# Kernel tuning notes

Hardware: AMD Instinct MI355X
Metric: run time of the kernel (lower is better)

The kernel has to match this reference:

```python
import jax, jax.numpy as jnp
import numpy as np

DECAY = 0.999
EPS = 1e-05
COMMIT = 0.25


def _layer_norm(x, g, b, eps=1e-5):
    mu = x.mean(-1, keepdims=True)
    var = ((x - mu) ** 2).mean(-1, keepdims=True)
    return (x - mu) * jax.lax.rsqrt(var + eps) * g + b


def setup_inputs() -> dict:
    key = jax.random.key(0)
    ks = jax.random.split(key, 8)
    B, T, D, M, H = 8, 4096, 512, 1024, 512
    init_bound = 1.0 / 512
    embedding = jax.random.uniform(ks[0], (M, D), jnp.float32, -init_bound, init_bound)
    return {
        "dense_x": jax.random.normal(ks[1], (B, T, D), jnp.float32),
        "dense_padding_mask": jax.random.randint(ks[2], (B, T), 0, 2).astype(bool),
        "labels": jax.random.randint(ks[3], (B, T), 0, M),
        "embedding": embedding,
        "ema_count": jnp.zeros((M,), jnp.float32),
        "ema_weight": embedding,
        "ln1_g": jnp.ones((D,), jnp.float32),
        "ln1_b": jnp.zeros((D,), jnp.float32),
        "W1": jax.random.normal(ks[4], (D, H), jnp.float32) * (1.0 / np.sqrt(D)),
        "ln2_g": jnp.ones((H,), jnp.float32),
        "ln2_b": jnp.zeros((H,), jnp.float32),
        "W2": jax.random.normal(ks[5], (H, M), jnp.float32) * (1.0 / np.sqrt(H)),
    }


def reference(dense_x, dense_padding_mask, labels, embedding, ema_count, ema_weight,
              ln1_g, ln1_b, W1, ln2_g, ln2_b, W2):
    B, T, D = dense_x.shape
    M = embedding.shape[0]
    N = B * T

    # ---- VQ codebook (EMA) ----
    x_flat = jax.lax.stop_gradient(dense_x).reshape(N, D)
    distances = (jnp.sum(embedding ** 2, axis=1)[None, :]
                 + jnp.sum(x_flat ** 2, axis=1, keepdims=True)
                 - 2.0 * (x_flat @ embedding.T))
    indices = jnp.argmin(distances, axis=-1)  # [N]
    quantized = embedding[indices].reshape(B, T, D)

    # EMA codebook update (training path); encodings.sum(0) and encodings.T @ x
    # expressed as scatter-adds instead of materializing [N, M] one-hot.
    counts = jnp.zeros((M,), dense_x.dtype).at[indices].add(1.0)
    new_count = DECAY * ema_count + (1.0 - DECAY) * counts
    n = jnp.sum(new_count)
    new_count = (new_count + EPS) / (n + M * EPS) * n
    dw = jnp.zeros((M, D), dense_x.dtype).at[indices].add(x_flat)
    new_weight = DECAY * ema_weight + (1.0 - DECAY) * dw
    new_embedding = new_weight / new_count[:, None]

    e_latent_loss = (dense_x - jax.lax.stop_gradient(quantized)) ** 2  # [B,T,D]
    vq_loss = COMMIT * e_latent_loss
    quantized_st = dense_x + jax.lax.stop_gradient(quantized - dense_x)

    avg_probs = counts / N
    perplexity = jnp.exp(-jnp.sum(avg_probs * jnp.log(avg_probs + 1e-10)))

    # ---- decoder: LN -> ReLU -> Linear -> LN -> ReLU -> Linear ----
    h = jax.nn.relu(_layer_norm(dense_x, ln1_g, ln1_b)) @ W1      # [B,T,H]
    logits = jax.nn.relu(_layer_norm(h, ln2_g, ln2_b)) @ W2       # [B,T,M]

    # ---- cross-entropy with ignore_index=-1 (padding) ----
    lab = jnp.where(dense_padding_mask, -1, labels)
    valid = lab >= 0
    safe = jnp.where(valid, lab, 0)
    logp = jax.nn.log_softmax(logits, axis=-1)
    ce = -jnp.take_along_axis(logp, safe[..., None], axis=-1)[..., 0]
    recon_loss = jnp.where(valid, ce, 0.0)

    loss = recon_loss + vq_loss.sum(-1)  # [B,T]
    return quantized_st, loss, perplexity, new_embedding, new_count, new_weight
```

## Files before the change

kernel.cpp:

```cpp
#include <hip/hip_runtime.h>


#define N_TOK 32768
#define WAITV(n) __builtin_amdgcn_s_waitcnt(0x0F70 | (n))
#define BAR() __builtin_amdgcn_s_barrier()

typedef __attribute__((ext_vector_type(8))) short short8;
typedef _Float16 half8 __attribute__((ext_vector_type(8)));
typedef __attribute__((ext_vector_type(4))) float f32x4;

__device__ __forceinline__ f32x4 mfma16(short8 a, short8 b, f32x4 c) {
    return __builtin_amdgcn_mfma_f32_16x16x32_bf16(a, b, c, 0, 0, 0);
}
__device__ __forceinline__ f32x4 mfma16h(half8 a, half8 b, f32x4 c) {
    return __builtin_amdgcn_mfma_f32_16x16x32_f16(a, b, c, 0, 0, 0);
}

__device__ __forceinline__ void gl_lds16(const unsigned short* g, char* l) {
    __builtin_amdgcn_global_load_lds(
        (const __attribute__((address_space(1))) void*)g,
        (__attribute__((address_space(3))) void*)l, 16, 0, 0);
}

__device__ __forceinline__ unsigned short f2bf(float x) {
    unsigned u = __float_as_uint(x);
    u += 0x7fffu + ((u >> 16) & 1u);
    return (unsigned short)(u >> 16);
}
__device__ __forceinline__ float bf2f(unsigned short h) {
    return __uint_as_float(((unsigned)h) << 16);
}
__device__ __forceinline__ unsigned short f2h(float x) {
    union { _Float16 h; unsigned short u; } c;
    c.h = (_Float16)x;
    return c.u;
}
__device__ __forceinline__ float h2f(unsigned short u) {
    union { _Float16 h; unsigned short u; } c;
    c.u = u;
    return (float)c.h;
}

__device__ __forceinline__ float waveSum(float v) {
#pragma unroll
    for (int off = 32; off > 0; off >>= 1) v += __shfl_down(v, off, 64);
    return v;
}
__device__ __forceinline__ float xorSum(float v) {
#pragma unroll
    for (int off = 1; off < 64; off <<= 1) v += __shfl_xor(v, off);
    return v;
}

__global__ __launch_bounds__(256) void prep_x_kernel(
        const float* __restrict__ X, const float* __restrict__ g,
        const float* __restrict__ b, unsigned short* __restrict__ Xf,
        unsigned short* __restrict__ A1, unsigned long long* __restrict__ minpack) {
    int tid = threadIdx.x;
    if (tid < 4) minpack[(blockIdx.x << 2) + tid] = ~0ULL;
    int lane = tid & 63;
    int n = (blockIdx.x << 2) + (tid >> 6);
    const float* row = X + ((size_t)n << 9);
    float v[8]; float s = 0.f, ss = 0.f;
#pragma unroll
    for (int i = 0; i < 8; ++i) { v[i] = row[lane + (i << 6)]; s += v[i]; ss += v[i] * v[i]; }
    s = xorSum(s); ss = xorSum(ss);
    float mu = s * (1.f / 512.f);
    float rs = rsqrtf(ss * (1.f / 512.f) - mu * mu + 1e-5f);
#pragma unroll
    for (int i = 0; i < 8; ++i) {
        int c = lane + (i << 6);
        size_t o = ((size_t)n << 9) + c;
        float x = v[i];
        Xf[o] = f2h(x);
        float a = fmaxf((x - mu) * rs * g[c] + b[c], 0.f);
        A1[o] = f2bf(a);
    }
}

__global__ __launch_bounds__(256) void prep_h_kernel(
        const unsigned short* __restrict__ Hb, const float* __restrict__ g,
        const float* __restrict__ b, unsigned short* __restrict__ A2) {
    int lane = threadIdx.x & 63;
    int n = (blockIdx.x << 2) + (threadIdx.x >> 6);
    const unsigned short* row = Hb + ((size_t)n << 9);
    float v[8]; float s = 0.f, ss = 0.f;
#pragma unroll
    for (int i = 0; i < 8; ++i) { v[i] = bf2f(row[lane + (i << 6)]); s += v[i]; ss += v[i] * v[i]; }
    s = xorSum(s); ss = xorSum(ss);
    float mu = s * (1.f / 512.f);
    float rs = rsqrtf(ss * (1.f / 512.f) - mu * mu + 1e-5f);
#pragma unroll
    for (int i = 0; i < 8; ++i) {
        int c = lane + (i << 6);
        float a = fmaxf((v[i] - mu) * rs * g[c] + b[c], 0.f);
        A2[((size_t)n << 9) + c] = f2bf(a);
    }
}

__global__ __launch_bounds__(256) void prep_e_kernel(
        const float* __restrict__ E, unsigned short* __restrict__ Ehf,
        unsigned short* __restrict__ Elf, float* __restrict__ e_sq,
        int* __restrict__ izero) {
    if (blockIdx.x < 8) izero[(blockIdx.x << 8) + threadIdx.x] = 0;
    int lane = threadIdx.x & 63;
    int m = (blockIdx.x << 2) + (threadIdx.x >> 6);
    const float* row = E + ((size_t)m << 9);
    float ss = 0.f;
#pragma unroll
    for (int i = 0; i < 8; ++i) {
        int c = lane + (i << 6);
        float x = row[c];
        ss += x * x;
        float xs = x * 512.f;
        unsigned short h = f2h(xs);
        size_t o = ((size_t)m << 9) + c;
        Ehf[o] = h;
        Elf[o] = f2h(xs - h2f(h));
    }
    ss = xorSum(ss);
    if (lane == 0) e_sq[m] = ss * 512.f;
}

__global__ __launch_bounds__(256) void prep_wt_kernel(
        const float* __restrict__ W1, const float* __restrict__ W2,
        unsigned short* __restrict__ W1T, unsigned short* __restrict__ W2T) {
    __shared__ float t[32][33];
    int bx = blockIdx.x;
    const float* W = (bx < 16) ? W1 : W2;
    unsigned short* WT = (bx < 16) ? W1T : W2T;
    int Nw = (bx < 16) ? 512 : 1024;
    int n0 = ((bx < 16) ? bx : (bx - 16)) << 5, k0 = blockIdx.y << 5;
    int tx = threadIdx.x & 31, ty = threadIdx.x >> 5;
#pragma unroll
    for (int l = 0; l < 4; ++l)
        t[ty + (l << 3)][tx] = W[(size_t)(k0 + ty + (l << 3)) * Nw + n0 + tx];
    __syncthreads();
#pragma unroll
    for (int l = 0; l < 4; ++l)
        WT[(((size_t)(n0 + ty + (l << 3))) << 9) + k0 + tx] = f2bf(t[tx][ty + (l << 3)]);
}

__device__ __forceinline__ unsigned long long packDist(float d, int m) {
    unsigned u = __float_as_uint(d);
    u = (u & 0x80000000u) ? ~u : (u | 0x80000000u);
    return ((unsigned long long)u << 32) | (unsigned)m;
}

__global__ __launch_bounds__(256) void dist_mfma_kernel(
        const unsigned short* __restrict__ Xf,
        const unsigned short* __restrict__ Ehf, const unsigned short* __restrict__ Elf,
        const float* __restrict__ e_sq, unsigned long long* __restrict__ minpack) {
    __shared__ __align__(16) short L[2][3][4096];
    int tid = threadIdx.x, lane = tid & 63, w = tid >> 6;
    int quad = lane >> 4, lanelo = lane & 15;
    int wm = w >> 1, wn = w & 1;
    int bid = blockIdx.x, xcd = bid & 7, s = bid >> 3;
    int row0 = (((s >> 3) << 3) | xcd) << 7;
    int m0 = (s & 7) << 7;

    int srow = ((w & 1) << 6) + lane;
    int skoff = (w >> 1) << 4;
    const unsigned short* pX = Xf  + (((size_t)(row0 + srow)) << 9) + skoff;
    const unsigned short* pH = Ehf + (((size_t)(m0  + srow)) << 9) + skoff;
    const unsigned short* pL = Elf + (((size_t)(m0  + srow)) << 9) + skoff;
    char* ldsB = (char*)&L[0][0][0] + ((w >> 1) << 12) + ((w & 1) << 10) + (lane << 4);
    const char* ra  = (const char*)&L[0][0][0] + (quad << 11) + (((wm << 6) + lanelo) << 4);
    const char* rbh = (const char*)&L[0][1][0] + (quad << 11) + (((wn << 6) + lanelo) << 4);

    f32x4 acc[4][4];
#pragma unroll
    for (int i = 0; i < 4; ++i)
#pragma unroll
        for (int j = 0; j < 4; ++j) acc[i][j] = 0.f;

    gl_lds16(pX, ldsB);            gl_lds16(pX + 8, ldsB + 2048);
    gl_lds16(pH, ldsB + 8192);     gl_lds16(pH + 8, ldsB + 10240);
    gl_lds16(pL, ldsB + 16384);    gl_lds16(pL + 8, ldsB + 18432);

#pragma unroll
    for (int it = 0; it < 16; ++it) {
        const int cb = it & 1;
        if (it < 15) {
            const unsigned short* sX = pX + ((it + 1) << 5);
            const unsigned short* sH = pH + ((it + 1) << 5);
            const unsigned short* sL = pL + ((it + 1) << 5);
            char* d = ldsB + (cb ^ 1) * 24576;
            gl_lds16(sX, d);           gl_lds16(sX + 8, d + 2048);
            gl_lds16(sH, d + 8192);    gl_lds16(sH + 8, d + 10240);
            gl_lds16(sL, d + 16384);   gl_lds16(sL + 8, d + 18432);
            WAITV(6);
        } else {
            WAITV(0);
        }
        BAR();
        const char* A  = ra  + cb * 24576;
        const char* Bh = rbh + cb * 24576;
        half8 av[4], bh[4], bl[4];
#pragma unroll
        for (int i = 0; i < 4; ++i) av[i] = *(const half8*)(A + (i << 8));
#pragma unroll
        for (int j = 0; j < 4; ++j) {
            bh[j] = *(const half8*)(Bh + (j << 8));
            bl[j] = *(const half8*)(Bh + 8192 + (j << 8));
        }
#pragma unroll
        for (int i = 0; i < 4; ++i)
#pragma unroll
            for (int j = 0; j < 4; ++j) acc[i][j] = mfma16h(av[i], bh[j], acc[i][j]);
#pragma unroll
        for (int i = 0; i < 4; ++i)
#pragma unroll
            for (int j = 0; j < 4; ++j) acc[i][j] = mfma16h(av[i], bl[j], acc[i][j]);
        BAR();
    }

    float esq[4];
#pragma unroll
    for (int j = 0; j < 4; ++j) esq[j] = e_sq[m0 + (wn << 6) + (j << 4) + lanelo];
#pragma unroll
    for (int i = 0; i < 4; ++i)
#pragma unroll
        for (int r = 0; r < 4; ++r) {
            unsigned long long best = ~0ULL;
#pragma unroll
            for (int j = 0; j < 4; ++j) {
                int code = m0 + (wn << 6) + (j << 4) + lanelo;
                float d = esq[j] - 2.f * acc[i][j][r];
                unsigned long long p = packDist(d, code);
                if (p < best) best = p;
            }
#pragma unroll
            for (int off = 1; off < 16; off <<= 1) {
                unsigned long long q = __shfl_xor(best, off);
                if (q < best) best = q;
            }
            if (lanelo == 0) {
                int t = row0 + (wm << 6) + (i << 4) + (quad << 2) + r;
                atomicMin(&minpack[t], best);
            }
        }
}

__global__ __launch_bounds__(256) void gather_kernel(
        const float* __restrict__ X, const float* __restrict__ E,
        const unsigned long long* __restrict__ minpack,
        float* __restrict__ out_q, int* __restrict__ icounts,
        float* __restrict__ vqsum) {
    int lane = threadIdx.x & 63;
    int n = (blockIdx.x << 2) + (threadIdx.x >> 6);
    int idx = (int)(minpack[n] & 0xFFFFFFFFULL);
    if (lane == 0) atomicAdd(&icounts[idx], 1);
    const float* xr = X + ((size_t)n << 9);
    const float* er = E + ((size_t)idx << 9);
    float s = 0.f;
#pragma unroll
    for (int i = 0; i < 8; ++i) {
        int c = lane + (i << 6);
        float xv = xr[c], q = er[c];
        out_q[((size_t)n << 9) + c] = q;
        float dlt = xv - q;
        s += dlt * dlt;
    }
    s = waveSum(s);
    if (lane == 0) vqsum[n] = 0.25f * s;
}

__global__ __launch_bounds__(1024) void codebook_kernel(
        const float* __restrict__ ema_count, const int* __restrict__ icounts,
        float* __restrict__ out_perp, float* __restrict__ out_newcount,
        int* __restrict__ offsets) {
    __shared__ int sc[1024];
    __shared__ float red[16];
    int tid = threadIdx.x;
    int lane = tid & 63, wid = tid >> 6;
    int ic = icounts[tid];
    sc[tid] = ic;
    for (int off = 1; off < 1024; off <<= 1) {
        __syncthreads();
        int v = (tid >= off) ? sc[tid - off] : 0;
        __syncthreads();
        sc[tid] += v;
    }
    offsets[tid] = sc[tid] - ic;
    __syncthreads();

    float cnt = (float)ic;
    float raw = 0.999f * ema_count[tid] + 0.001f * cnt;
    float v = waveSum(raw);
    if (lane == 0) red[wid] = v;
    __syncthreads();
    float nsum = 0.f;
#pragma unroll
    for (int i = 0; i < 16; ++i) nsum += red[i];
    __syncthreads();
    float p = cnt * (1.f / 32768.f);
    float e = p * logf(p + 1e-10f);
    e = waveSum(e);
    if (lane == 0) red[wid] = e;
    __syncthreads();
    float ent = 0.f;
#pragma unroll
    for (int i = 0; i < 16; ++i) ent += red[i];
    float nc = (raw + 1e-5f) / (nsum + 1024.f * 1e-5f) * nsum;
    out_newcount[tid] = nc;
    if (tid == 0) out_perp[0] = expf(-ent);
}

__global__ __launch_bounds__(256) void scatter_kernel(
        const unsigned long long* __restrict__ minpack,
        const int* __restrict__ offsets, int* __restrict__ cursor,
        int* __restrict__ bucket) {
    int n = (blockIdx.x << 8) + threadIdx.x;
    int idx = (int)(minpack[n] & 0xFFFFFFFFULL);
    int pos = atomicAdd(&cursor[idx], 1);
    bucket[offsets[idx] + pos] = n;
}

__global__ __launch_bounds__(256) void dw_kernel(
        const float* __restrict__ X, const int* __restrict__ bucket,
        const int* __restrict__ icounts, const int* __restrict__ offsets,
        float* __restrict__ dw) {
    __shared__ float comb[4][512];
    int tid = threadIdx.x, lane = tid & 63, w = tid >> 6;
    int m = blockIdx.x;
    int cnt = icounts[m], base = offsets[m];
    float acc[8] = {};
    for (int i = w; i < cnt; i += 4) {
        int t = bucket[base + i];
        const float* xr = X + ((size_t)t << 9);
#pragma unroll
        for (int j = 0; j < 8; ++j) acc[j] += xr[lane + (j << 6)];
    }
#pragma unroll
    for (int j = 0; j < 8; ++j) comb[w][lane + (j << 6)] = acc[j];
    __syncthreads();
    for (int c = tid; c < 512; c += 256)
        dw[((size_t)m << 9) + c] = comb[0][c] + comb[1][c] + comb[2][c] + comb[3][c];
}

__global__ __launch_bounds__(256) void gemm1_mfma_kernel(
        const unsigned short* __restrict__ A1, const unsigned short* __restrict__ W1T,
        unsigned short* __restrict__ Hb) {
    __shared__ __align__(16) short L[2][2][8192];
    int tid = threadIdx.x, lane = tid & 63, w = tid >> 6;
    int quad = lane >> 4, lanelo = lane & 15;
    int wm = w >> 1, wn = w & 1;
    int bid = blockIdx.x, xcd = bid & 7, s = bid >> 3;
    int row0 = (((s >> 2) << 3) | xcd) << 7;
    int n0 = (s & 3) << 7;

    int srow = ((w & 1) << 6) + lane;
    int skoff = (w >> 1) << 5;
    const unsigned short* pA = A1  + (((size_t)(row0 + srow)) << 9) + skoff;
    const unsigned short* pB = W1T + (((size_t)(n0   + srow)) << 9) + skoff;
    char* ldsB = (char*)&L[0][0][0] + ((w >> 1) << 13) + ((w & 1) << 10) + (lane << 4);
    const char* ra = (const char*)&L[0][0][0] + (quad << 11) + (((wm << 6) + lanelo) << 4);
    const char* rb = (const char*)&L[0][0][0] + 16384 + (quad << 11) + (((wn << 6) + lanelo) << 4);

    f32x4 acc[4][4];
#pragma unroll
    for (int i = 0; i < 4; ++i)
#pragma unroll
        for (int j = 0; j < 4; ++j) acc[i][j] = 0.f;

    gl_lds16(pA, ldsB);           gl_lds16(pA + 8, ldsB + 2048);
    gl_lds16(pA + 16, ldsB + 4096); gl_lds16(pA + 24, ldsB + 6144);
    gl_lds16(pB, ldsB + 16384);   gl_lds16(pB + 8, ldsB + 18432);
    gl_lds16(pB + 16, ldsB + 20480); gl_lds16(pB + 24, ldsB + 22528);

#pragma unroll
    for (int it = 0; it < 8; ++it) {
        const int cb = it & 1;
        if (it < 7) {
            const unsigned short* sA = pA + ((it + 1) << 6);
            const unsigned short* sB = pB + ((it + 1) << 6);
            char* d = ldsB + (cb ^ 1) * 32768;
            gl_lds16(sA, d);           gl_lds16(sA + 8, d + 2048);
            gl_lds16(sA + 16, d + 4096); gl_lds16(sA + 24, d + 6144);
            gl_lds16(sB, d + 16384);   gl_lds16(sB + 8, d + 18432);
            gl_lds16(sB + 16, d + 20480); gl_lds16(sB + 24, d + 22528);
            WAITV(8);
        } else {
            WAITV(0);
        }
        BAR();
        const char* A = ra + cb * 32768;
        const char* B = rb + cb * 32768;
#pragma unroll
        for (int kk = 0; kk < 2; ++kk) {
            short8 af[4], bf4[4];
#pragma unroll
            for (int i = 0; i < 4; ++i) af[i] = *(const short8*)(A + (kk << 13) + (i << 8));
#pragma unroll
            for (int j = 0; j < 4; ++j) bf4[j] = *(const short8*)(B + (kk << 13) + (j << 8));
#pragma unroll
            for (int i = 0; i < 4; ++i)
#pragma unroll
                for (int j = 0; j < 4; ++j) acc[i][j] = mfma16(af[i], bf4[j], acc[i][j]);
        }
        BAR();
    }
#pragma unroll
    for (int i = 0; i < 4; ++i)
#pragma unroll
        for (int j = 0; j < 4; ++j)
#pragma unroll
            for (int r = 0; r < 4; ++r) {
                int row = row0 + (wm << 6) + (i << 4) + (quad << 2) + r;
                int col = n0 + (wn << 6) + (j << 4) + lanelo;
                Hb[((size_t)row << 9) + col] = f2bf(acc[i][j][r]);
            }
}

__global__ __launch_bounds__(256) void gemm2_chunk_kernel(
        const unsigned short* __restrict__ A2, const unsigned short* __restrict__ W2T,
        const int* __restrict__ mask, const int* __restrict__ labels,
        float* __restrict__ ws_cmax, float* __restrict__ ws_csum,
        float* __restrict__ ws_lab) {
    __shared__ __align__(16) short L[2][2][8192];
    __shared__ float lmax[2][2][64], lsum[2][2][64], llab[128];
    __shared__ int slab[128];
    int tid = threadIdx.x, lane = tid & 63, w = tid >> 6;
    int quad = lane >> 4, lanelo = lane & 15;
    int wm = w >> 1, wn = w & 1;
    int bid = blockIdx.x, xcd = bid & 7, s = bid >> 3;
    int row0 = (((s >> 3) << 3) | xcd) << 7;
    int cy = s & 7;
    int c0 = cy << 7;
    if (tid < 128) {
        int mk = mask[row0 + tid];
        slab[tid] = mk ? 0 : labels[row0 + tid];
    }
    __syncthreads();

    int srow = ((w & 1) << 6) + lane;
    int skoff = (w >> 1) << 5;
    const unsigned short* pA = A2  + (((size_t)(row0 + srow)) << 9) + skoff;
    const unsigned short* pB = W2T + (((size_t)(c0   + srow)) << 9) + skoff;
    char* ldsB = (char*)&L[0][0][0] + ((w >> 1) << 13) + ((w & 1) << 10) + (lane << 4);
    const char* ra = (const char*)&L[0][0][0] + (quad << 11) + (((wm << 6) + lanelo) << 4);
    const char* rb = (const char*)&L[0][0][0] + 16384 + (quad << 11) + (((wn << 6) + lanelo) << 4);

    f32x4 acc[4][4];
#pragma unroll
    for (int i = 0; i < 4; ++i)
#pragma unroll
        for (int j = 0; j < 4; ++j) acc[i][j] = 0.f;

    gl_lds16(pA, ldsB);           gl_lds16(pA + 8, ldsB + 2048);
    gl_lds16(pA + 16, ldsB + 4096); gl_lds16(pA + 24, ldsB + 6144);
    gl_lds16(pB, ldsB + 16384);   gl_lds16(pB + 8, ldsB + 18432);
    gl_lds16(pB + 16, ldsB + 20480); gl_lds16(pB + 24, ldsB + 22528);

#pragma unroll
    for (int it = 0; it < 8; ++it) {
        const int cb = it & 1;
        if (it < 7) {
            const unsigned short* sA = pA + ((it + 1) << 6);
            const unsigned short* sB = pB + ((it + 1) << 6);
            char* d = ldsB + (cb ^ 1) * 32768;
            gl_lds16(sA, d);           gl_lds16(sA + 8, d + 2048);
            gl_lds16(sA + 16, d + 4096); gl_lds16(sA + 24, d + 6144);
            gl_lds16(sB, d + 16384);   gl_lds16(sB + 8, d + 18432);
            gl_lds16(sB + 16, d + 20480); gl_lds16(sB + 24, d + 22528);
            WAITV(8);
        } else {
            WAITV(0);
        }
        BAR();
        const char* A = ra + cb * 32768;
        const char* B = rb + cb * 32768;
#pragma unroll
        for (int kk = 0; kk < 2; ++kk) {
            short8 af[4], bf4[4];
#pragma unroll
            for (int i = 0; i < 4; ++i) af[i] = *(const short8*)(A + (kk << 13) + (i << 8));
#pragma unroll
            for (int j = 0; j < 4; ++j) bf4[j] = *(const short8*)(B + (kk << 13) + (j << 8));
#pragma unroll
            for (int i = 0; i < 4; ++i)
#pragma unroll
                for (int j = 0; j < 4; ++j) acc[i][j] = mfma16(af[i], bf4[j], acc[i][j]);
        }
        BAR();
    }

#pragma unroll
    for (int i = 0; i < 4; ++i)
#pragma unroll
        for (int j = 0; j < 4; ++j)
#pragma unroll
            for (int r = 0; r < 4; ++r) {
                int code = c0 + (wn << 6) + (j << 4) + lanelo;
                int tt = (wm << 6) + (i << 4) + (quad << 2) + r;
                if (code == slab[tt]) llab[tt] = acc[i][j][r];
            }
#pragma unroll
    for (int i = 0; i < 4; ++i)
#pragma unroll
        for (int r = 0; r < 4; ++r) {
            float mx = fmaxf(fmaxf(acc[i][0][r], acc[i][1][r]),
                             fmaxf(acc[i][2][r], acc[i][3][r]));
#pragma unroll
            for (int off = 1; off < 16; off <<= 1) mx = fmaxf(mx, __shfl_xor(mx, off));
            if (lanelo == 0) lmax[wm][wn][(i << 4) + (quad << 2) + r] = mx;
        }
    __syncthreads();
#pragma unroll
    for (int i = 0; i < 4; ++i)
#pragma unroll
        for (int r = 0; r < 4; ++r) {
            int tl = (i << 4) + (quad << 2) + r;
            float cm = fmaxf(lmax[wm][0][tl], lmax[wm][1][tl]);
            float s2 = expf(acc[i][0][r] - cm) + expf(acc[i][1][r] - cm) +
                       expf(acc[i][2][r] - cm) + expf(acc[i][3][r] - cm);
#pragma unroll
            for (int off = 1; off < 16; off <<= 1) s2 += __shfl_xor(s2, off);
            if (lanelo == 0) lsum[wm][wn][tl] = s2;
        }
    __syncthreads();
    if (tid < 128) {
        int wmi = tid >> 6, tl = tid & 63;
        int token = row0 + tid;
        float cm = fmaxf(lmax[wmi][0][tl], lmax[wmi][1][tl]);
        float cs = lsum[wmi][0][tl] + lsum[wmi][1][tl];
        size_t o = ((size_t)cy << 15) + token;
        ws_cmax[o] = cm;
        ws_csum[o] = cs;
        if ((slab[tid] >> 7) == cy) ws_lab[token] = llab[tid];
    }
}

__global__ __launch_bounds__(256) void epilogue_kernel(
        const float* __restrict__ ema_weight, const float* __restrict__ dw,
        const float* __restrict__ newcount, float* __restrict__ out_neww,
        float* __restrict__ out_newemb,
        const float* __restrict__ ws_cmax, const float* __restrict__ ws_csum,
        const float* __restrict__ ws_lab, const int* __restrict__ mask,
        const float* __restrict__ vqsum, float* __restrict__ loss_out) {
    int bx = blockIdx.x;
    if (bx < 2048) {
        int i = (bx << 8) + threadIdx.x;
        float nw = 0.999f * ema_weight[i] + 0.001f * dw[i];
        out_neww[i] = nw;
        out_newemb[i] = nw / newcount[i >> 9];
    } else {
        int n = ((bx - 2048) << 8) + threadIdx.x;
        float m[8], s[8];
#pragma unroll
        for (int c = 0; c < 8; ++c) {
            m[c] = ws_cmax[(c << 15) + n];
            s[c] = ws_csum[(c << 15) + n];
        }
        float gm = m[0];
#pragma unroll
        for (int c = 1; c < 8; ++c) gm = fmaxf(gm, m[c]);
        float se = 0.f;
#pragma unroll
        for (int c = 0; c < 8; ++c) se += s[c] * expf(m[c] - gm);
        float ce = -(ws_lab[n] - gm - logf(se));
        loss_out[n] = (mask[n] ? 0.f : ce) + vqsum[n];
    }
}

extern "C" void kernel_launch(void* const* d_in, const int* in_sizes, int n_in,
                              void* d_out, int out_size, void* d_ws, size_t ws_size,
                              hipStream_t stream) {
    const float* X          = (const float*)d_in[0];
    const int*   mask       = (const int*)d_in[1];
    const int*   labels     = (const int*)d_in[2];
    const float* E          = (const float*)d_in[3];
    const float* ema_count  = (const float*)d_in[4];
    const float* ema_weight = (const float*)d_in[5];
    const float* g1 = (const float*)d_in[6];
    const float* b1 = (const float*)d_in[7];
    const float* W1 = (const float*)d_in[8];
    const float* g2 = (const float*)d_in[9];
    const float* b2 = (const float*)d_in[10];
    const float* W2 = (const float*)d_in[11];

    float* out = (float*)d_out;
    float* out_q        = out;
    float* out_loss     = out + 16777216;
    float* out_perp     = out + 16809984;
    float* out_newemb   = out + 16809985;
    float* out_newcount = out + 17334273;
    float* out_neww     = out + 17335297;

    float* w = (float*)d_ws;
    float* vqsum = w;  w += 32768;
    float* e_sq = w;   w += 1024;
    float* dwbuf = w;  w += 524288;
    unsigned long long* minpack = (unsigned long long*)w; w += 65536;
    float* ws_cmax = w; w += 262144;
    float* ws_csum = w; w += 262144;
    float* ws_lab  = w; w += 32768;
    int* icounts = (int*)w; w += 1024;
    int* cursor  = (int*)w; w += 1024;
    int* offsets = (int*)w; w += 1024;
    int* bucket  = (int*)w; w += 32768;
    unsigned short* Ehf = (unsigned short*)w; w += 262144;
    unsigned short* Elf = (unsigned short*)w; w += 262144;
    unsigned short* W1T = (unsigned short*)w; w += 131072;
    unsigned short* W2T = (unsigned short*)w; w += 262144;
    unsigned short* Xf  = (unsigned short*)w; w += 8388608;
    unsigned short* A1  = (unsigned short*)w; w += 8388608;
    unsigned short* Hb  = (unsigned short*)w; w += 8388608;
    unsigned short* A2  = Xf;

    prep_e_kernel<<<256, 256, 0, stream>>>(E, Ehf, Elf, e_sq, icounts);
    prep_wt_kernel<<<dim3(48, 16), 256, 0, stream>>>(W1, W2, W1T, W2T);
    prep_x_kernel<<<8192, 256, 0, stream>>>(X, g1, b1, Xf, A1, minpack);
    dist_mfma_kernel<<<2048, 256, 0, stream>>>(Xf, Ehf, Elf, e_sq, minpack);
    gather_kernel<<<8192, 256, 0, stream>>>(X, E, minpack, out_q, icounts, vqsum);
    codebook_kernel<<<1, 1024, 0, stream>>>(ema_count, icounts, out_perp,
                                            out_newcount, offsets);
    scatter_kernel<<<128, 256, 0, stream>>>(minpack, offsets, cursor, bucket);
    dw_kernel<<<1024, 256, 0, stream>>>(X, bucket, icounts, offsets, dwbuf);
    gemm1_mfma_kernel<<<1024, 256, 0, stream>>>(A1, W1T, Hb);
    prep_h_kernel<<<8192, 256, 0, stream>>>(Hb, g2, b2, A2);
    gemm2_chunk_kernel<<<2048, 256, 0, stream>>>(A2, W2T, mask, labels,
                                                 ws_cmax, ws_csum, ws_lab);
    epilogue_kernel<<<2176, 256, 0, stream>>>(ema_weight, dwbuf, out_newcount,
                                              out_neww, out_newemb,
                                              ws_cmax, ws_csum, ws_lab,
                                              mask, vqsum, out_loss);
}
```

Measured before the change: 477.2 us.

## Horizontally fuse independent kernels into shared launches with block-role dispatch

```diff
diff --git a/kernel.cpp b/kernel.cpp
--- a/kernel.cpp
+++ b/kernel.cpp
@@ -78,26 +78,6 @@
     }
 }
 
-__global__ __launch_bounds__(256) void prep_h_kernel(
-        const unsigned short* __restrict__ Hb, const float* __restrict__ g,
-        const float* __restrict__ b, unsigned short* __restrict__ A2) {
-    int lane = threadIdx.x & 63;
-    int n = (blockIdx.x << 2) + (threadIdx.x >> 6);
-    const unsigned short* row = Hb + ((size_t)n << 9);
-    float v[8]; float s = 0.f, ss = 0.f;
-#pragma unroll
-    for (int i = 0; i < 8; ++i) { v[i] = bf2f(row[lane + (i << 6)]); s += v[i]; ss += v[i] * v[i]; }
-    s = xorSum(s); ss = xorSum(ss);
-    float mu = s * (1.f / 512.f);
-    float rs = rsqrtf(ss * (1.f / 512.f) - mu * mu + 1e-5f);
-#pragma unroll
-    for (int i = 0; i < 8; ++i) {
-        int c = lane + (i << 6);
-        float a = fmaxf((v[i] - mu) * rs * g[c] + b[c], 0.f);
-        A2[((size_t)n << 9) + c] = f2bf(a);
-    }
-}
-
 __global__ __launch_bounds__(256) void prep_e_kernel(
         const float* __restrict__ E, unsigned short* __restrict__ Ehf,
         unsigned short* __restrict__ Elf, float* __restrict__ e_sq,
@@ -147,26 +127,25 @@
     return ((unsigned long long)u << 32) | (unsigned)m;
 }
 
-__global__ __launch_bounds__(256) void dist_mfma_kernel(
+__device__ __forceinline__ void dist_body(
+        int q, int x, char* LB,
         const unsigned short* __restrict__ Xf,
         const unsigned short* __restrict__ Ehf, const unsigned short* __restrict__ Elf,
         const float* __restrict__ e_sq, unsigned long long* __restrict__ minpack) {
-    __shared__ __align__(16) short L[2][3][4096];
     int tid = threadIdx.x, lane = tid & 63, w = tid >> 6;
     int quad = lane >> 4, lanelo = lane & 15;
     int wm = w >> 1, wn = w & 1;
-    int bid = blockIdx.x, xcd = bid & 7, s = bid >> 3;
-    int row0 = (((s >> 3) << 3) | xcd) << 7;
-    int m0 = (s & 7) << 7;
+    int row0 = (((q >> 3) << 3) | x) << 7;
+    int m0 = (q & 7) << 7;
 
     int srow = ((w & 1) << 6) + lane;
     int skoff = (w >> 1) << 4;
     const unsigned short* pX = Xf  + (((size_t)(row0 + srow)) << 9) + skoff;
     const unsigned short* pH = Ehf + (((size_t)(m0  + srow)) << 9) + skoff;
     const unsigned short* pL = Elf + (((size_t)(m0  + srow)) << 9) + skoff;
-    char* ldsB = (char*)&L[0][0][0] + ((w >> 1) << 12) + ((w & 1) << 10) + (lane << 4);
-    const char* ra  = (const char*)&L[0][0][0] + (quad << 11) + (((wm << 6) + lanelo) << 4);
-    const char* rbh = (const char*)&L[0][1][0] + (quad << 11) + (((wn << 6) + lanelo) << 4);
+    char* ldsB = LB + ((w >> 1) << 12) + ((w & 1) << 10) + (lane << 4);
+    const char* ra  = LB + (quad << 11) + (((wm << 6) + lanelo) << 4);
+    const char* rbh = LB + 8192 + (quad << 11) + (((wn << 6) + lanelo) << 4);
 
     f32x4 acc[4][4];
 #pragma unroll
@@ -232,8 +211,8 @@
             }
 #pragma unroll
             for (int off = 1; off < 16; off <<= 1) {
-                unsigned long long q = __shfl_xor(best, off);
-                if (q < best) best = q;
+                unsigned long long q2 = __shfl_xor(best, off);
+                if (q2 < best) best = q2;
             }
             if (lanelo == 0) {
                 int t = row0 + (wm << 6) + (i << 4) + (quad << 2) + r;
@@ -242,28 +221,133 @@
         }
 }
 
-__global__ __launch_bounds__(256) void gather_kernel(
+__device__ __forceinline__ void gemm1_body(
+        int g, int x, char* LB,
+        const unsigned short* __restrict__ A1, const unsigned short* __restrict__ W1T,
+        unsigned short* __restrict__ Hb) {
+    int tid = threadIdx.x, lane = tid & 63, w = tid >> 6;
+    int quad = lane >> 4, lanelo = lane & 15;
+    int wm = w >> 1, wn = w & 1;
+    int row0 = (((g >> 2) << 3) | x) << 7;
+    int n0 = (g & 3) << 7;
+
+    int srow = ((w & 1) << 6) + lane;
+    int skoff = (w >> 1) << 5;
+    const unsigned short* pA = A1  + (((size_t)(row0 + srow)) << 9) + skoff;
+    const unsigned short* pB = W1T + (((size_t)(n0   + srow)) << 9) + skoff;
+    char* ldsB = LB + ((w >> 1) << 13) + ((w & 1) << 10) + (lane << 4);
+    const char* ra = LB + (quad << 11) + (((wm << 6) + lanelo) << 4);
+    const char* rb = LB + 16384 + (quad << 11) + (((wn << 6) + lanelo) << 4);
+
+    f32x4 acc[4][4];
+#pragma unroll
+    for (int i = 0; i < 4; ++i)
+#pragma unroll
+        for (int j = 0; j < 4; ++j) acc[i][j] = 0.f;
+
+    gl_lds16(pA, ldsB);           gl_lds16(pA + 8, ldsB + 2048);
+    gl_lds16(pA + 16, ldsB + 4096); gl_lds16(pA + 24, ldsB + 6144);
+    gl_lds16(pB, ldsB + 16384);   gl_lds16(pB + 8, ldsB + 18432);
+    gl_lds16(pB + 16, ldsB + 20480); gl_lds16(pB + 24, ldsB + 22528);
+
+#pragma unroll
+    for (int it = 0; it < 8; ++it) {
+        const int cb = it & 1;
+        if (it < 7) {
+            const unsigned short* sA = pA + ((it + 1) << 6);
+            const unsigned short* sB = pB + ((it + 1) << 6);
+            char* d = ldsB + (cb ^ 1) * 32768;
+            gl_lds16(sA, d);           gl_lds16(sA + 8, d + 2048);
+            gl_lds16(sA + 16, d + 4096); gl_lds16(sA + 24, d + 6144);
+            gl_lds16(sB, d + 16384);   gl_lds16(sB + 8, d + 18432);
+            gl_lds16(sB + 16, d + 20480); gl_lds16(sB + 24, d + 22528);
+            WAITV(8);
+        } else {
+            WAITV(0);
+        }
+        BAR();
+        const char* A = ra + cb * 32768;
+        const char* B = rb + cb * 32768;
+#pragma unroll
+        for (int kk = 0; kk < 2; ++kk) {
+            short8 af[4], bf4[4];
+#pragma unroll
+            for (int i = 0; i < 4; ++i) af[i] = *(const short8*)(A + (kk << 13) + (i << 8));
+#pragma unroll
+            for (int j = 0; j < 4; ++j) bf4[j] = *(const short8*)(B + (kk << 13) + (j << 8));
+#pragma unroll
+            for (int i = 0; i < 4; ++i)
+#pragma unroll
+                for (int j = 0; j < 4; ++j) acc[i][j] = mfma16(af[i], bf4[j], acc[i][j]);
+        }
+        BAR();
+    }
+#pragma unroll
+    for (int i = 0; i < 4; ++i)
+#pragma unroll
+        for (int j = 0; j < 4; ++j)
+#pragma unroll
+            for (int r = 0; r < 4; ++r) {
+                int row = row0 + (wm << 6) + (i << 4) + (quad << 2) + r;
+                int col = n0 + (wn << 6) + (j << 4) + lanelo;
+                Hb[((size_t)row << 9) + col] = f2bf(acc[i][j][r]);
+            }
+}
+
+__global__ __launch_bounds__(256) void fused1_kernel(
+        const unsigned short* __restrict__ Xf,
+        const unsigned short* __restrict__ Ehf, const unsigned short* __restrict__ Elf,
+        const float* __restrict__ e_sq, unsigned long long* __restrict__ minpack,
+        const unsigned short* __restrict__ A1, const unsigned short* __restrict__ W1T,
+        unsigned short* __restrict__ Hb) {
+    __shared__ __align__(16) char LB[65536];
+    int b = blockIdx.x, x = b & 7, m = b >> 3;
+    int t = m % 3, g = m / 3;
+    if (t < 2) dist_body((g << 1) + t, x, LB, Xf, Ehf, Elf, e_sq, minpack);
+    else       gemm1_body(g, x, LB, A1, W1T, Hb);
+}
+
+__global__ __launch_bounds__(256) void fused2_kernel(
         const float* __restrict__ X, const float* __restrict__ E,
         const unsigned long long* __restrict__ minpack,
         float* __restrict__ out_q, int* __restrict__ icounts,
-        float* __restrict__ vqsum) {
+        float* __restrict__ vqsum,
+        const unsigned short* __restrict__ Hb, const float* __restrict__ g2,
+        const float* __restrict__ b2, unsigned short* __restrict__ A2) {
+    int nb = blockIdx.x >> 1;
     int lane = threadIdx.x & 63;
-    int n = (blockIdx.x << 2) + (threadIdx.x >> 6);
-    int idx = (int)(minpack[n] & 0xFFFFFFFFULL);
-    if (lane == 0) atomicAdd(&icounts[idx], 1);
-    const float* xr = X + ((size_t)n << 9);
-    const float* er = E + ((size_t)idx << 9);
-    float s = 0.f;
-#pragma unroll
-    for (int i = 0; i < 8; ++i) {
-        int c = lane + (i << 6);
-        float xv = xr[c], q = er[c];
-        out_q[((size_t)n << 9) + c] = q;
-        float dlt = xv - q;
-        s += dlt * dlt;
-    }
-    s = waveSum(s);
-    if (lane == 0) vqsum[n] = 0.25f * s;
+    int n = (nb << 2) + (threadIdx.x >> 6);
+    if ((blockIdx.x & 1) == 0) {
+        int idx = (int)(minpack[n] & 0xFFFFFFFFULL);
+        if (lane == 0) atomicAdd(&icounts[idx], 1);
+        const float* xr = X + ((size_t)n << 9);
+        const float* er = E + ((size_t)idx << 9);
+        float s = 0.f;
+#pragma unroll
+        for (int i = 0; i < 8; ++i) {
+            int c = lane + (i << 6);
+            float xv = xr[c], q = er[c];
+            out_q[((size_t)n << 9) + c] = q;
+            float dlt = xv - q;
+            s += dlt * dlt;
+        }
+        s = waveSum(s);
+        if (lane == 0) vqsum[n] = 0.25f * s;
+    } else {
+        const unsigned short* row = Hb + ((size_t)n << 9);
+        float v[8]; float s = 0.f, ss = 0.f;
+#pragma unroll
+        for (int i = 0; i < 8; ++i) { v[i] = bf2f(row[lane + (i << 6)]); s += v[i]; ss += v[i] * v[i]; }
+        s = xorSum(s); ss = xorSum(ss);
+        float mu = s * (1.f / 512.f);
+        float rs = rsqrtf(ss * (1.f / 512.f) - mu * mu + 1e-5f);
+#pragma unroll
+        for (int i = 0; i < 8; ++i) {
+            int c = lane + (i << 6);
+            float a = fmaxf((v[i] - mu) * rs * g2[c] + b2[c], 0.f);
+            A2[((size_t)n << 9) + c] = f2bf(a);
+        }
+    }
 }
 
 __global__ __launch_bounds__(1024) void codebook_kernel(
@@ -317,13 +401,12 @@
     bucket[offsets[idx] + pos] = n;
 }
 
-__global__ __launch_bounds__(256) void dw_kernel(
-        const float* __restrict__ X, const int* __restrict__ bucket,
-        const int* __restrict__ icounts, const int* __restrict__ offsets,
-        float* __restrict__ dw) {
-    __shared__ float comb[4][512];
+__device__ __forceinline__ void dw_body(
+        int m, char* LB, const float* __restrict__ X,
+        const int* __restrict__ bucket, const int* __restrict__ icounts,
+        const int* __restrict__ offsets, float* __restrict__ dw) {
+    float* comb = (float*)LB;
     int tid = threadIdx.x, lane = tid & 63, w = tid >> 6;
-    int m = blockIdx.x;
     int cnt = icounts[m], base = offsets[m];
     float acc[8] = {};
     for (int i = w; i < cnt; i += 4) {
@@ -333,30 +416,38 @@
         for (int j = 0; j < 8; ++j) acc[j] += xr[lane + (j << 6)];
     }
 #pragma unroll
-    for (int j = 0; j < 8; ++j) comb[w][lane + (j << 6)] = acc[j];
+    for (int j = 0; j < 8; ++j) comb[(w << 9) + lane + (j << 6)] = acc[j];
     __syncthreads();
     for (int c = tid; c < 512; c += 256)
-        dw[((size_t)m << 9) + c] = comb[0][c] + comb[1][c] + comb[2][c] + comb[3][c];
-}
-
-__global__ __launch_bounds__(256) void gemm1_mfma_kernel(
-        const unsigned short* __restrict__ A1, const unsigned short* __restrict__ W1T,
-        unsigned short* __restrict__ Hb) {
-    __shared__ __align__(16) short L[2][2][8192];
+        dw[((size_t)m << 9) + c] = comb[c] + comb[512 + c] + comb[1024 + c] + comb[1536 + c];
+}
+
+__device__ __forceinline__ void gemm2_body(
+        int q, int x, char* LB,
+        float (*lmax)[2][64], float (*lsum)[2][64], float* llab, int* slab,
+        const unsigned short* __restrict__ A2, const unsigned short* __restrict__ W2T,
+        const int* __restrict__ mask, const int* __restrict__ labels,
+        float* __restrict__ ws_cmax, float* __restrict__ ws_csum,
+        float* __restrict__ ws_lab) {
     int tid = threadIdx.x, lane = tid & 63, w = tid >> 6;
     int quad = lane >> 4, lanelo = lane & 15;
     int wm = w >> 1, wn = w & 1;
-    int bid = blockIdx.x, xcd = bid & 7, s = bid >> 3;
-    int row0 = (((s >> 2) << 3) | xcd) << 7;
-    int n0 = (s & 3) << 7;
+    int row0 = (((q >> 3) << 3) | x) << 7;
+    int cy = q & 7;
+    int c0 = cy << 7;
+    if (tid < 128) {
+        int mk = mask[row0 + tid];
+        slab[tid] = mk ? 0 : labels[row0 + tid];
+    }
+    __syncthreads();
 
     int srow = ((w & 1) << 6) + lane;
     int skoff = (w >> 1) << 5;
-    const unsigned short* pA = A1  + (((size_t)(row0 + srow)) << 9) + skoff;
-    const unsigned short* pB = W1T + (((size_t)(n0   + srow)) << 9) + skoff;
-    char* ldsB = (char*)&L[0][0][0] + ((w >> 1) << 13) + ((w & 1) << 10) + (lane << 4);
-    const char* ra = (const char*)&L[0][0][0] + (quad << 11) + (((wm << 6) + lanelo) << 4);
-    const char* rb = (const char*)&L[0][0][0] + 16384 + (quad << 11) + (((wn << 6) + lanelo) << 4);
+    const unsigned short* pA = A2  + (((size_t)(row0 + srow)) << 9) + skoff;
+    const unsigned short* pB = W2T + (((size_t)(c0   + srow)) << 9) + skoff;
+    char* ldsB = LB + ((w >> 1) << 13) + ((w & 1) << 10) + (lane << 4);
+    const char* ra = LB + (quad << 11) + (((wm << 6) + lanelo) << 4);
+    const char* rb = LB + 16384 + (quad << 11) + (((wn << 6) + lanelo) << 4);
 
     f32x4 acc[4][4];
 #pragma unroll
@@ -401,90 +492,6 @@
         }
         BAR();
     }
-#pragma unroll
-    for (int i = 0; i < 4; ++i)
-#pragma unroll
-        for (int j = 0; j < 4; ++j)
-#pragma unroll
-            for (int r = 0; r < 4; ++r) {
-                int row = row0 + (wm << 6) + (i << 4) + (quad << 2) + r;
-                int col = n0 + (wn << 6) + (j << 4) + lanelo;
-                Hb[((size_t)row << 9) + col] = f2bf(acc[i][j][r]);
-            }
-}
-
-__global__ __launch_bounds__(256) void gemm2_chunk_kernel(
-        const unsigned short* __restrict__ A2, const unsigned short* __restrict__ W2T,
-        const int* __restrict__ mask, const int* __restrict__ labels,
-        float* __restrict__ ws_cmax, float* __restrict__ ws_csum,
-        float* __restrict__ ws_lab) {
-    __shared__ __align__(16) short L[2][2][8192];
-    __shared__ float lmax[2][2][64], lsum[2][2][64], llab[128];
-    __shared__ int slab[128];
-    int tid = threadIdx.x, lane = tid & 63, w = tid >> 6;
-    int quad = lane >> 4, lanelo = lane & 15;
-    int wm = w >> 1, wn = w & 1;
-    int bid = blockIdx.x, xcd = bid & 7, s = bid >> 3;
-    int row0 = (((s >> 3) << 3) | xcd) << 7;
-    int cy = s & 7;
-    int c0 = cy << 7;
-    if (tid < 128) {
-        int mk = mask[row0 + tid];
-        slab[tid] = mk ? 0 : labels[row0 + tid];
-    }
-    __syncthreads();
-
-    int srow = ((w & 1) << 6) + lane;
-    int skoff = (w >> 1) << 5;
-    const unsigned short* pA = A2  + (((size_t)(row0 + srow)) << 9) + skoff;
-    const unsigned short* pB = W2T + (((size_t)(c0   + srow)) << 9) + skoff;
-    char* ldsB = (char*)&L[0][0][0] + ((w >> 1) << 13) + ((w & 1) << 10) + (lane << 4);
-    const char* ra = (const char*)&L[0][0][0] + (quad << 11) + (((wm << 6) + lanelo) << 4);
-    const char* rb = (const char*)&L[0][0][0] + 16384 + (quad << 11) + (((wn << 6) + lanelo) << 4);
-
-    f32x4 acc[4][4];
-#pragma unroll
-    for (int i = 0; i < 4; ++i)
-#pragma unroll
-        for (int j = 0; j < 4; ++j) acc[i][j] = 0.f;
-
-    gl_lds16(pA, ldsB);           gl_lds16(pA + 8, ldsB + 2048);
-    gl_lds16(pA + 16, ldsB + 4096); gl_lds16(pA + 24, ldsB + 6144);
-    gl_lds16(pB, ldsB + 16384);   gl_lds16(pB + 8, ldsB + 18432);
-    gl_lds16(pB + 16, ldsB + 20480); gl_lds16(pB + 24, ldsB + 22528);
-
-#pragma unroll
-    for (int it = 0; it < 8; ++it) {
-        const int cb = it & 1;
-        if (it < 7) {
-            const unsigned short* sA = pA + ((it + 1) << 6);
-            const unsigned short* sB = pB + ((it + 1) << 6);
-            char* d = ldsB + (cb ^ 1) * 32768;
-            gl_lds16(sA, d);           gl_lds16(sA + 8, d + 2048);
-            gl_lds16(sA + 16, d + 4096); gl_lds16(sA + 24, d + 6144);
-            gl_lds16(sB, d + 16384);   gl_lds16(sB + 8, d + 18432);
-            gl_lds16(sB + 16, d + 20480); gl_lds16(sB + 24, d + 22528);
-            WAITV(8);
-        } else {
-            WAITV(0);
-        }
-        BAR();
-        const char* A = ra + cb * 32768;
-        const char* B = rb + cb * 32768;
-#pragma unroll
-        for (int kk = 0; kk < 2; ++kk) {
-            short8 af[4], bf4[4];
-#pragma unroll
-            for (int i = 0; i < 4; ++i) af[i] = *(const short8*)(A + (kk << 13) + (i << 8));
-#pragma unroll
-            for (int j = 0; j < 4; ++j) bf4[j] = *(const short8*)(B + (kk << 13) + (j << 8));
-#pragma unroll
-            for (int i = 0; i < 4; ++i)
-#pragma unroll
-                for (int j = 0; j < 4; ++j) acc[i][j] = mfma16(af[i], bf4[j], acc[i][j]);
-        }
-        BAR();
-    }
 
 #pragma unroll
     for (int i = 0; i < 4; ++i)
@@ -530,6 +537,24 @@
         ws_csum[o] = cs;
         if ((slab[tid] >> 7) == cy) ws_lab[token] = llab[tid];
     }
+}
+
+__global__ __launch_bounds__(256) void fused3_kernel(
+        const unsigned short* __restrict__ A2, const unsigned short* __restrict__ W2T,
+        const int* __restrict__ mask, const int* __restrict__ labels,
+        float* __restrict__ ws_cmax, float* __restrict__ ws_csum,
+        float* __restrict__ ws_lab,
+        const float* __restrict__ X, const int* __restrict__ bucket,
+        const int* __restrict__ icounts, const int* __restrict__ offsets,
+        float* __restrict__ dw) {
+    __shared__ __align__(16) char LB[65536];
+    __shared__ float lmax[2][2][64], lsum[2][2][64], llab[128];
+    __shared__ int slab[128];
+    int b = blockIdx.x, x = b & 7, m = b >> 3;
+    int t = m % 3, g = m / 3;
+    if (t < 2) gemm2_body((g << 1) + t, x, LB, lmax, lsum, llab, slab,
+                          A2, W2T, mask, labels, ws_cmax, ws_csum, ws_lab);
+    else       dw_body((g << 3) | x, LB, X, bucket, icounts, offsets, dw);
 }
 
 __global__ __launch_bounds__(256) void epilogue_kernel(
@@ -612,16 +637,16 @@
     prep_e_kernel<<<256, 256, 0, stream>>>(E, Ehf, Elf, e_sq, icounts);
     prep_wt_kernel<<<dim3(48, 16), 256, 0, stream>>>(W1, W2, W1T, W2T);
     prep_x_kernel<<<8192, 256, 0, stream>>>(X, g1, b1, Xf, A1, minpack);
-    dist_mfma_kernel<<<2048, 256, 0, stream>>>(Xf, Ehf, Elf, e_sq, minpack);
-    gather_kernel<<<8192, 256, 0, stream>>>(X, E, minpack, out_q, icounts, vqsum);
+    fused1_kernel<<<3072, 256, 0, stream>>>(Xf, Ehf, Elf, e_sq, minpack,
+                                            A1, W1T, Hb);
+    fused2_kernel<<<16384, 256, 0, stream>>>(X, E, minpack, out_q, icounts,
+                                             vqsum, Hb, g2, b2, A2);
     codebook_kernel<<<1, 1024, 0, stream>>>(ema_count, icounts, out_perp,
                                             out_newcount, offsets);
     scatter_kernel<<<128, 256, 0, stream>>>(minpack, offsets, cursor, bucket);
-    dw_kernel<<<1024, 256, 0, stream>>>(X, bucket, icounts, offsets, dwbuf);
-    gemm1_mfma_kernel<<<1024, 256, 0, stream>>>(A1, W1T, Hb);
-    prep_h_kernel<<<8192, 256, 0, stream>>>(Hb, g2, b2, A2);
-    gemm2_chunk_kernel<<<2048, 256, 0, stream>>>(A2, W2T, mask, labels,
-                                                 ws_cmax, ws_csum, ws_lab);
+    fused3_kernel<<<3072, 256, 0, stream>>>(A2, W2T, mask, labels,
+                                            ws_cmax, ws_csum, ws_lab,
+                                            X, bucket, icounts, offsets, dwbuf);
     epilogue_kernel<<<2176, 256, 0, stream>>>(ema_weight, dwbuf, out_newcount,
                                               out_neww, out_newemb,
                                               ws_cmax, ws_csum, ws_lab,
```

Measured after the change: 480.5 us. About the same (+0.7%).
